# Kernel optimization log

Hardware: AMD Instinct MI355X
Metric: run time of the kernel (lower is better)

## Reference

```python
import jax, jax.numpy as jnp
import numpy as np


def setup_inputs() -> dict:
    key = jax.random.key(0)
    k1, k2, k3 = jax.random.split(key, 3)
    B, S, C, D, V = 16, 2048, 16, 256, 100000
    value_seq = jax.random.randint(k1, (B, S, C), 0, V, dtype=jnp.int64)
    hidden = jax.random.normal(k2, (B, S, D), dtype=jnp.float32)
    value_table = jax.random.normal(k3, (V, D), dtype=jnp.float32)
    return {"value_seq": value_seq, "hidden": hidden, "value_table": value_table}


def reference(value_seq, hidden, value_table):
    # padding_idx=0: row 0 of the embedding table is zeros
    table = value_table.at[0].set(0.0)
    # gather: [B,S,C,D]
    value_embed = table[value_seq]
    # dot attention scores over the C context slots: [B,S,C]
    u = jnp.einsum('bsd,bscd->bsc', hidden, value_embed)
    p = jax.nn.softmax(u, axis=-1)
    # weighted combine: [B,S,D]
    o = jnp.einsum('bsc,bscd->bsd', p, value_embed)
    return o
```

## Files before the change

kernel.cpp:

```cpp
#include <hip/hip_runtime.h>


#define KV_C 16
#define KV_D 256
#define KV_TOKENS (16 * 2048)

__global__ __launch_bounds__(256, 2) void kv_mem_kernel(
    const int* __restrict__ seq,
    const float* __restrict__ hidden,
    const float* __restrict__ table,
    float* __restrict__ out)
{
    const int wave = threadIdx.x >> 6;
    const int lane = threadIdx.x & 63;
    const int token = blockIdx.x * 4 + wave;

    const float4 h = *(const float4*)(hidden + (size_t)token * KV_D + lane * 4);

    const int* sp = seq + (size_t)token * KV_C;
    int myidx = (lane < KV_C) ? sp[lane] : 0;

    float4 e[KV_C];

    #pragma unroll
    for (int c = 0; c < KV_C; ++c) {
        int idx = __shfl(myidx, c);
        float4 ev = make_float4(0.f, 0.f, 0.f, 0.f);
        if (idx != 0) {
            ev = *(const float4*)(table + (size_t)idx * KV_D + lane * 4);
        }
        e[c] = ev;
    }

    #pragma unroll
    for (int c = 0; c < KV_C; ++c) {
        asm volatile("" : "+v"(e[c].x), "+v"(e[c].y), "+v"(e[c].z), "+v"(e[c].w));
    }

    float u[KV_C];
    #pragma unroll
    for (int c = 0; c < KV_C; ++c) {
        u[c] = h.x * e[c].x + h.y * e[c].y + h.z * e[c].z + h.w * e[c].w;
    }

    #pragma unroll
    for (int s = 32; s >= 1; s >>= 1) {
        #pragma unroll
        for (int c = 0; c < KV_C; ++c) {
            u[c] += __shfl_xor(u[c], s);
        }
    }

    float m = u[0];
    #pragma unroll
    for (int c = 1; c < KV_C; ++c) m = fmaxf(m, u[c]);
    float sum = 0.f;
    #pragma unroll
    for (int c = 0; c < KV_C; ++c) {
        u[c] = __expf(u[c] - m);
        sum += u[c];
    }
    const float inv = 1.0f / sum;

    float4 o = make_float4(0.f, 0.f, 0.f, 0.f);
    #pragma unroll
    for (int c = 0; c < KV_C; ++c) {
        const float w = u[c] * inv;
        o.x += w * e[c].x;
        o.y += w * e[c].y;
        o.z += w * e[c].z;
        o.w += w * e[c].w;
    }

    *(float4*)(out + (size_t)token * KV_D + lane * 4) = o;
}

extern "C" void kernel_launch(void* const* d_in, const int* in_sizes, int n_in,
                              void* d_out, int out_size, void* d_ws, size_t ws_size,
                              hipStream_t stream) {
    const int*   seq    = (const int*)d_in[0];
    const float* hidden = (const float*)d_in[1];
    const float* table  = (const float*)d_in[2];
    float*       out    = (float*)d_out;

    dim3 grid(KV_TOKENS / 4);
    dim3 block(256);
    kv_mem_kernel<<<grid, block, 0, stream>>>(seq, hidden, table, out);
}
```

Measured before the change: 229.3 us.

## Gather embedding rows straight into LDS with global_load_lds and mask padding rows

The table-row gather now uses async global-to-LDS loads instead of holding all 16 float4 rows in VGPRs. Both the score and the combine loops read the rows back from LDS. Padding index 0 is handled with a ballot mask rather than a branch around each load. Blocks shrink to 128 threads with 2 tokens each. The aim is to free registers and keep more gather requests in flight, at the cost of 32KB of LDS per block, extra LDS reads, and an LDS-limited occupancy.

```diff
diff --git a/kernel.cpp b/kernel.cpp
--- a/kernel.cpp
+++ b/kernel.cpp
@@ -1,46 +1,55 @@
 #include <hip/hip_runtime.h>
+#include <stdint.h>
 
 
 #define KV_C 16
 #define KV_D 256
 #define KV_TOKENS (16 * 2048)
+#define TOK_PER_BLK 2
 
-__global__ __launch_bounds__(256, 2) void kv_mem_kernel(
+typedef __attribute__((address_space(3))) void       lds_void;
+typedef const __attribute__((address_space(1))) void gbl_void;
+
+__global__ __launch_bounds__(128) void kv_mem_kernel(
     const int* __restrict__ seq,
     const float* __restrict__ hidden,
     const float* __restrict__ table,
     float* __restrict__ out)
 {
+    __shared__ float smem[TOK_PER_BLK * KV_C * KV_D];
+
     const int wave = threadIdx.x >> 6;
     const int lane = threadIdx.x & 63;
-    const int token = blockIdx.x * 4 + wave;
+    const int token = blockIdx.x * TOK_PER_BLK + wave;
+
+    float* lbase = smem + wave * (KV_C * KV_D);
+
+    const int* sp = seq + (size_t)token * KV_C;
+    int myidx = (lane < KV_C) ? sp[lane] : 0;
+    const unsigned long long nz = __ballot(myidx != 0);
+
+    int idxs[KV_C];
+    #pragma unroll
+    for (int c = 0; c < KV_C; ++c) idxs[c] = __shfl(myidx, c);
 
     const float4 h = *(const float4*)(hidden + (size_t)token * KV_D + lane * 4);
 
-    const int* sp = seq + (size_t)token * KV_C;
-    int myidx = (lane < KV_C) ? sp[lane] : 0;
-
-    float4 e[KV_C];
-
     #pragma unroll
     for (int c = 0; c < KV_C; ++c) {
-        int idx = __shfl(myidx, c);
-        float4 ev = make_float4(0.f, 0.f, 0.f, 0.f);
-        if (idx != 0) {
-            ev = *(const float4*)(table + (size_t)idx * KV_D + lane * 4);
-        }
-        e[c] = ev;
+        const float* gp = table + (size_t)idxs[c] * KV_D + lane * 4;
+        __builtin_amdgcn_global_load_lds((gbl_void*)gp,
+                                         (lds_void*)(lbase + c * KV_D),
+                                         16, 0, 0);
     }
 
-    #pragma unroll
-    for (int c = 0; c < KV_C; ++c) {
-        asm volatile("" : "+v"(e[c].x), "+v"(e[c].y), "+v"(e[c].z), "+v"(e[c].w));
-    }
+    asm volatile("s_waitcnt vmcnt(0)" ::: "memory");
 
     float u[KV_C];
     #pragma unroll
     for (int c = 0; c < KV_C; ++c) {
-        u[c] = h.x * e[c].x + h.y * e[c].y + h.z * e[c].z + h.w * e[c].w;
+        const float4 ev = *(const float4*)(lbase + c * KV_D + lane * 4);
+        const float msk = ((nz >> c) & 1ULL) ? 1.0f : 0.0f;
+        u[c] = msk * (h.x * ev.x + h.y * ev.y + h.z * ev.z + h.w * ev.w);
     }
 
     #pragma unroll
@@ -65,11 +74,13 @@
     float4 o = make_float4(0.f, 0.f, 0.f, 0.f);
     #pragma unroll
     for (int c = 0; c < KV_C; ++c) {
-        const float w = u[c] * inv;
-        o.x += w * e[c].x;
-        o.y += w * e[c].y;
-        o.z += w * e[c].z;
-        o.w += w * e[c].w;
+        const float4 ev = *(const float4*)(lbase + c * KV_D + lane * 4);
+        const float msk = ((nz >> c) & 1ULL) ? 1.0f : 0.0f;
+        const float w = u[c] * inv * msk;
+        o.x += w * ev.x;
+        o.y += w * ev.y;
+        o.z += w * ev.z;
+        o.w += w * ev.w;
     }
 
     *(float4*)(out + (size_t)token * KV_D + lane * 4) = o;
@@ -83,7 +94,7 @@
     const float* table  = (const float*)d_in[2];
     float*       out    = (float*)d_out;
 
-    dim3 grid(KV_TOKENS / 4);
-    dim3 block(256);
+    dim3 grid(KV_TOKENS / TOK_PER_BLK);
+    dim3 block(128);
     kv_mem_kernel<<<grid, block, 0, stream>>>(seq, hidden, table, out);
 }
```

After: 244.0 us. 6.4% more time.
